# Optimization experiments

Hardware: AMD Instinct MI355X
Metric: run time of the kernel (lower is better)

The kernel has to match this reference:

```python
import jax, jax.numpy as jnp
import numpy as np

N_HARMONIC = 6
CONCAT = (3,)  # cfg.append_distance: concat embedding after this layer index
N_LAYERS = 8


def harmonic_embedding(x):
    # x: [N, 3] -> [N, 6*2*3 + 3] = [N, 39]
    freqs = 2.0 ** jnp.arange(N_HARMONIC, dtype=x.dtype)  # omega0 = 1.0, logspace
    embed = (x[..., None] * freqs).reshape(*x.shape[:-1], -1)  # [N, 18]
    return jnp.concatenate([jnp.sin(embed), jnp.cos(embed), x], axis=-1)


def setup_inputs() -> dict:
    key = jax.random.key(0)
    N, H, E = 262144, 256, 39
    ks = jax.random.split(key, 11)
    inp = {"points": jax.random.normal(ks[0], (N, 3), dtype=jnp.float32)}
    in_dims = [E, H, H, H, E + H, H, H, H]  # skip-concat before layer 4
    for i, d_in in enumerate(in_dims):
        scale = 1.0 / np.sqrt(d_in)
        inp[f"w{i}"] = jax.random.normal(ks[i + 1], (d_in, H), dtype=jnp.float32) * scale
        inp[f"b{i}"] = jnp.zeros((H,), dtype=jnp.float32)
    inp["wsdf"] = jax.random.normal(ks[9], (H, 1), dtype=jnp.float32) * (1.0 / np.sqrt(H))
    inp["bsdf"] = jnp.zeros((1,), dtype=jnp.float32)
    return inp


def reference(points, w0, b0, w1, b1, w2, b2, w3, b3, w4, b4, w5, b5, w6, b6, w7, b7, wsdf, bsdf):
    ws = [w0, w1, w2, w3, w4, w5, w6, w7]
    bs = [b0, b1, b2, b3, b4, b5, b6, b7]
    emb = harmonic_embedding(points.reshape(-1, 3))  # [N, 39]
    x = emb
    for i in range(N_LAYERS):
        x = jax.nn.relu(x @ ws[i] + bs[i])
        if i in CONCAT:
            x = jnp.concatenate([emb, x], axis=-1)  # torch.cat([add, xyz])
    return x @ wsdf + bsdf  # [N, 1] signed distance
```

## Files before the change

kernel.cpp:

```cpp
#include <hip/hip_runtime.h>
#include <hip/hip_fp16.h>

typedef _Float16 f16x8 __attribute__((ext_vector_type(8)));
typedef _Float16 f16x4 __attribute__((ext_vector_type(4)));
typedef _Float16 f16x2 __attribute__((ext_vector_type(2)));
typedef float    f32x16 __attribute__((ext_vector_type(16)));
typedef float    f32x4 __attribute__((ext_vector_type(4)));

#define SH 264
#define SE 56
#define PTS 64

struct LayerPtrs {
  const float* w[8];
  const float* b[8];
};

__global__ void prep_weights(LayerPtrs P, f16x8* __restrict__ wf) {
  int gid = blockIdx.x * 256 + threadIdx.x;
  if (gid >= 60416) return;
  const int OFF[9] = {0,1536,9728,17920,26112,35840,44032,52224,60416};
  int l = 0;
  while (gid >= OFF[l+1]) ++l;
  int f = gid - OFF[l];
  int lane = f & 63;
  int t = f >> 6;
  int mtile = t & 7;
  int kc = t >> 3;
  int col = mtile * 32 + (lane & 31);
  int kb  = (lane >> 5) * 8;
  const float* w = P.w[l];
  f16x8 v;
#pragma unroll
  for (int j = 0; j < 8; ++j) {
    float x = 0.f;
    if (l == 4) {
      if (kc < 3) {
        int k = kc * 16 + kb + j;
        if (k < 39) x = w[k * 256 + col];
      } else {
        int k = (kc - 3) * 16 + kb + j;
        x = w[(39 + k) * 256 + col];
      }
    } else if (l == 0) {
      int k = kc * 16 + kb + j;
      if (k < 39) x = w[k * 256 + col];
    } else {
      int k = kc * 16 + kb + j;
      x = w[k * 256 + col];
    }
    v[j] = (_Float16)x;
  }
  wf[gid] = v;
}

#define MFMA __builtin_amdgcn_mfma_f32_32x32x16_f16

__device__ __forceinline__ void aload2(f16x8& d0, f16x8& d1, const f16x8* p) {
  asm volatile("global_load_dwordx4 %0, %2, off\n\t"
               "global_load_dwordx4 %1, %2, off offset:1024"
               : "=&v"(d0), "=&v"(d1)
               : "v"(p));
}

__device__ __forceinline__ void mfma4(f16x8 a0, f16x8 a1, f16x8 v0, f16x8 v1,
                                      f32x16 acc[2][2]) {
  acc[0][0] = MFMA(a0, v0, acc[0][0], 0, 0, 0);
  acc[0][1] = MFMA(a0, v1, acc[0][1], 0, 0, 0);
  acc[1][0] = MFMA(a1, v0, acc[1][0], 0, 0, 0);
  acc[1][1] = MFMA(a1, v1, acc[1][1], 0, 0, 0);
}

__device__ __forceinline__ void mfma4_z(f16x8 a0, f16x8 a1, f16x8 v0, f16x8 v1,
                                        f32x16 acc[2][2]) {
  const f32x16 z = {};
  acc[0][0] = MFMA(a0, v0, z, 0, 0, 0);
  acc[0][1] = MFMA(a0, v1, z, 0, 0, 0);
  acc[1][0] = MFMA(a1, v0, z, 0, 0, 0);
  acc[1][1] = MFMA(a1, v1, z, 0, 0, 0);
}

template<int NKC, bool FIRST, int RSTRIDE>
__device__ __forceinline__ void mm(const f16x8* __restrict__ wb,
                                   const char* __restrict__ r0,
                                   f32x16 acc[2][2]) {
  f16x8 a00, a01, b00, b01, c00, c01;
  aload2(a00, a01, wb);
  if (NKC > 1) aload2(b00, b01, wb + 512);
  if (NKC > 2) aload2(c00, c01, wb + 1024);
  f16x8 v0 = *(const f16x8*)(r0);
  f16x8 v1 = *(const f16x8*)(r0 + RSTRIDE);
#pragma unroll
  for (int kc = 0; kc < NKC; ++kc) {
    f16x8 na0, na1, nv0, nv1;
    if (kc + 3 < NKC) aload2(na0, na1, wb + (kc + 3) * 512);
    if (kc + 1 < NKC) {
      const char* rp = r0 + 32 * (kc + 1);
      nv0 = *(const f16x8*)(rp);
      nv1 = *(const f16x8*)(rp + RSTRIDE);
    }
    if (kc + 3 < NKC)      asm volatile("s_waitcnt vmcnt(6)");
    else if (kc + 2 < NKC) asm volatile("s_waitcnt vmcnt(4)");
    else if (kc + 1 < NKC) asm volatile("s_waitcnt vmcnt(2)");
    else                   asm volatile("s_waitcnt vmcnt(0)");
    __builtin_amdgcn_sched_barrier(0);
    if (FIRST && kc == 0) mfma4_z(a00, a01, v0, v1, acc);
    else                  mfma4 (a00, a01, v0, v1, acc);
    if (kc + 1 < NKC) {
      a00 = b00; a01 = b01; b00 = c00; b01 = c01;
      v0 = nv0; v1 = nv1;
    }
    if (kc + 3 < NKC) { c00 = na0; c01 = na1; }
  }
}

__device__ __forceinline__ f16x4 relu_cvt4(float a0, float a1, float a2, float a3) {
  f16x2 lo = __builtin_bit_cast(f16x2, __builtin_amdgcn_cvt_pkrtz(a0, a1));
  f16x2 hi = __builtin_bit_cast(f16x2, __builtin_amdgcn_cvt_pkrtz(a2, a3));
  union { f16x4 v; f16x2 h[2]; } u;
  u.h[0] = lo; u.h[1] = hi;
  f16x4 z = {};
  return __builtin_elementwise_max(u.v, z);
}

__device__ __forceinline__ void store_epi(f32x16 acc[2][2],
                                          const float* __restrict__ bias,
                                          int wg, int p0, int h,
                                          _Float16* __restrict__ Hw) {
#pragma unroll
  for (int mt = 0; mt < 2; ++mt) {
    int hb = wg * 64 + mt * 32 + 4 * h;
#pragma unroll
    for (int g = 0; g < 4; ++g) {
      f32x4 q = *(const f32x4*)&bias[hb + 8 * g];
#pragma unroll
      for (int nt = 0; nt < 2; ++nt) {
        f16x4 o = relu_cvt4(acc[mt][nt][4 * g + 0] + q[0],
                            acc[mt][nt][4 * g + 1] + q[1],
                            acc[mt][nt][4 * g + 2] + q[2],
                            acc[mt][nt][4 * g + 3] + q[3]);
        *(f16x4*)&Hw[(nt * 32 + p0) * SH + hb + 8 * g] = o;
      }
    }
  }
}

__device__ __forceinline__ void emb_channel(_Float16* __restrict__ Erow,
                                            int c, float x) {
  _Float16 sv[6], cv[6];
  float fr = 1.f;
#pragma unroll
  for (int k = 0; k < 6; ++k) {
    float e = x * fr;
    sv[k] = (_Float16)__sinf(e);
    cv[k] = (_Float16)__cosf(e);
    fr *= 2.f;
  }
#pragma unroll
  for (int k = 0; k < 6; k += 2) {
    f16x2 s2 = {sv[k], sv[k + 1]};
    f16x2 c2 = {cv[k], cv[k + 1]};
    *(f16x2*)&Erow[6 * c + k]      = s2;
    *(f16x2*)&Erow[18 + 6 * c + k] = c2;
  }
  Erow[36 + c] = (_Float16)x;
}

__global__ __launch_bounds__(256, 2)
void mlp_fused(const float* __restrict__ points,
               LayerPtrs P,
               const f16x8* __restrict__ wf,
               const float* __restrict__ wsdf,
               const float* __restrict__ bsdf,
               float* __restrict__ out) {
  __shared__ __align__(16) _Float16 Hs0[PTS * SH];
  __shared__ __align__(16) _Float16 Hs1[PTS * SH];
  __shared__ __align__(16) _Float16 Es[PTS * SE];
  const int tid = threadIdx.x;
  const int blk = blockIdx.x;

  const int lane = tid & 63;
  const int wg   = tid >> 6;
  const int p0   = lane & 31;
  const int h    = lane >> 5;

  const f16x8* wb = wf + wg * 128 + lane;

  {
    int p = tid & 63, part = tid >> 6;
    _Float16* Erow = &Es[p * SE];
    if (part < 3) {
      emb_channel(Erow, part, points[(blk * PTS + p) * 3 + part]);
    } else {
      Erow[39] = (_Float16)0.f;
      f16x4 z4 = {};
      *(f16x4*)&Erow[40] = z4;
      *(f16x4*)&Erow[44] = z4;
      *(f16x4*)&Erow[48] = z4;
      *(f16x4*)&Erow[52] = z4;
    }
  }
  __syncthreads();

  const char* h0R = (const char*)Hs0 + (p0 * SH + 8 * h) * 2;
  const char* h1R = (const char*)Hs1 + (p0 * SH + 8 * h) * 2;
  const char* eR  = (const char*)Es  + (p0 * SE + 8 * h) * 2;

  f32x16 acc[2][2];
  const int WOFF[8] = {0, 1536, 9728, 17920, 26112, 35840, 44032, 52224};

  mm<3, true, 32 * SE * 2>(wb, eR, acc);
  store_epi(acc, P.b[0], wg, p0, h, Hs0);
  __syncthreads();
  mm<16, true, 32 * SH * 2>(wb + WOFF[1], h0R, acc);
  store_epi(acc, P.b[1], wg, p0, h, Hs1);
  __syncthreads();
  mm<16, true, 32 * SH * 2>(wb + WOFF[2], h1R, acc);
  store_epi(acc, P.b[2], wg, p0, h, Hs0);
  __syncthreads();
  mm<16, true, 32 * SH * 2>(wb + WOFF[3], h0R, acc);
  store_epi(acc, P.b[3], wg, p0, h, Hs1);
  __syncthreads();
  mm<3, true, 32 * SE * 2>(wb + 26112, eR, acc);
  mm<16, false, 32 * SH * 2>(wb + 27648, h1R, acc);
  store_epi(acc, P.b[4], wg, p0, h, Hs0);
  __syncthreads();
  mm<16, true, 32 * SH * 2>(wb + WOFF[5], h0R, acc);
  store_epi(acc, P.b[5], wg, p0, h, Hs1);
  __syncthreads();
  mm<16, true, 32 * SH * 2>(wb + WOFF[6], h1R, acc);
  store_epi(acc, P.b[6], wg, p0, h, Hs0);
  __syncthreads();
  mm<16, true, 32 * SH * 2>(wb + WOFF[7], h0R, acc);
  {
    float part0 = 0.f, part1 = 0.f;
    const float* b7 = P.b[7];
#pragma unroll
    for (int mt = 0; mt < 2; ++mt) {
#pragma unroll
      for (int g = 0; g < 4; ++g) {
        int idx = wg * 64 + mt * 32 + 8 * g + 4 * h;
        f32x4 qb = *(const f32x4*)&b7[idx];
        f32x4 qw = *(const f32x4*)&wsdf[idx];
#pragma unroll
        for (int r = 0; r < 4; ++r) {
          part0 += fmaxf(acc[mt][0][4 * g + r] + qb[r], 0.f) * qw[r];
          part1 += fmaxf(acc[mt][1][4 * g + r] + qb[r], 0.f) * qw[r];
        }
      }
    }
    float* PB = (float*)Es;
    PB[(wg * 2 + h) * 64 + p0]      = part0;
    PB[(wg * 2 + h) * 64 + 32 + p0] = part1;
    __syncthreads();
    if (tid < PTS) {
      float s = bsdf[0];
#pragma unroll
      for (int j = 0; j < 8; ++j) s += PB[j * 64 + tid];
      out[blk * PTS + tid] = s;
    }
  }
}

extern "C" void kernel_launch(void* const* d_in, const int* in_sizes, int n_in,
                              void* d_out, int out_size, void* d_ws, size_t ws_size,
                              hipStream_t stream) {
  const float* points = (const float*)d_in[0];
  LayerPtrs P;
  for (int i = 0; i < 8; ++i) {
    P.w[i] = (const float*)d_in[1 + 2 * i];
    P.b[i] = (const float*)d_in[2 + 2 * i];
  }
  const float* wsdf = (const float*)d_in[17];
  const float* bsdf = (const float*)d_in[18];
  f16x8* wf = (f16x8*)d_ws;

  int N = in_sizes[0] / 3;
  prep_weights<<<236, 256, 0, stream>>>(P, wf);
  mlp_fused<<<N / PTS, 256, 0, stream>>>(points, P, wf, wsdf, bsdf, (float*)d_out);
}
```

Measured before the change: 318.6 us.

## Single-buffer activation LDS and raise occupancy to three blocks per CU

Replaces the ping-pong pair of activation buffers with one shared buffer, adding an extra barrier between each layer's matmul reads and the epilogue writes. This cuts LDS per block roughly in half so launch bounds can request three blocks per SM/CU instead of two. The cost is one more __syncthreads per layer, which serialises compute and store within a block, and a tighter register budget that may cause spills.

```diff
diff --git a/kernel.cpp b/kernel.cpp
--- a/kernel.cpp
+++ b/kernel.cpp
@@ -126,7 +126,7 @@
 __device__ __forceinline__ void store_epi(f32x16 acc[2][2],
                                           const float* __restrict__ bias,
                                           int wg, int p0, int h,
-                                          _Float16* __restrict__ Hw) {
+                                          _Float16* __restrict__ Hs) {
 #pragma unroll
   for (int mt = 0; mt < 2; ++mt) {
     int hb = wg * 64 + mt * 32 + 4 * h;
@@ -139,7 +139,7 @@
                             acc[mt][nt][4 * g + 1] + q[1],
                             acc[mt][nt][4 * g + 2] + q[2],
                             acc[mt][nt][4 * g + 3] + q[3]);
-        *(f16x4*)&Hw[(nt * 32 + p0) * SH + hb + 8 * g] = o;
+        *(f16x4*)&Hs[(nt * 32 + p0) * SH + hb + 8 * g] = o;
       }
     }
   }
@@ -166,15 +166,14 @@
   Erow[36 + c] = (_Float16)x;
 }
 
-__global__ __launch_bounds__(256, 2)
+__global__ __launch_bounds__(256, 3)
 void mlp_fused(const float* __restrict__ points,
                LayerPtrs P,
                const f16x8* __restrict__ wf,
                const float* __restrict__ wsdf,
                const float* __restrict__ bsdf,
                float* __restrict__ out) {
-  __shared__ __align__(16) _Float16 Hs0[PTS * SH];
-  __shared__ __align__(16) _Float16 Hs1[PTS * SH];
+  __shared__ __align__(16) _Float16 Hs[PTS * SH];
   __shared__ __align__(16) _Float16 Es[PTS * SE];
   const int tid = threadIdx.x;
   const int blk = blockIdx.x;
@@ -202,36 +201,41 @@
   }
   __syncthreads();
 
-  const char* h0R = (const char*)Hs0 + (p0 * SH + 8 * h) * 2;
-  const char* h1R = (const char*)Hs1 + (p0 * SH + 8 * h) * 2;
-  const char* eR  = (const char*)Es  + (p0 * SE + 8 * h) * 2;
+  const char* hR = (const char*)Hs + (p0 * SH + 8 * h) * 2;
+  const char* eR = (const char*)Es + (p0 * SE + 8 * h) * 2;
 
   f32x16 acc[2][2];
   const int WOFF[8] = {0, 1536, 9728, 17920, 26112, 35840, 44032, 52224};
 
   mm<3, true, 32 * SE * 2>(wb, eR, acc);
-  store_epi(acc, P.b[0], wg, p0, h, Hs0);
+  store_epi(acc, P.b[0], wg, p0, h, Hs);
   __syncthreads();
-  mm<16, true, 32 * SH * 2>(wb + WOFF[1], h0R, acc);
-  store_epi(acc, P.b[1], wg, p0, h, Hs1);
-  __syncthreads();
-  mm<16, true, 32 * SH * 2>(wb + WOFF[2], h1R, acc);
-  store_epi(acc, P.b[2], wg, p0, h, Hs0);
-  __syncthreads();
-  mm<16, true, 32 * SH * 2>(wb + WOFF[3], h0R, acc);
-  store_epi(acc, P.b[3], wg, p0, h, Hs1);
-  __syncthreads();
-  mm<3, true, 32 * SE * 2>(wb + 26112, eR, acc);
-  mm<16, false, 32 * SH * 2>(wb + 27648, h1R, acc);
-  store_epi(acc, P.b[4], wg, p0, h, Hs0);
-  __syncthreads();
-  mm<16, true, 32 * SH * 2>(wb + WOFF[5], h0R, acc);
-  store_epi(acc, P.b[5], wg, p0, h, Hs1);
-  __syncthreads();
-  mm<16, true, 32 * SH * 2>(wb + WOFF[6], h1R, acc);
-  store_epi(acc, P.b[6], wg, p0, h, Hs0);
-  __syncthreads();
-  mm<16, true, 32 * SH * 2>(wb + WOFF[7], h0R, acc);
+
+#pragma unroll
+  for (int l = 1; l < 4; ++l) {
+    mm<16, true, 32 * SH * 2>(wb + WOFF[l], hR, acc);
+    __syncthreads();
+    store_epi(acc, P.b[l], wg, p0, h, Hs);
+    __syncthreads();
+  }
+
+  {
+    mm<3, true, 32 * SE * 2>(wb + 26112, eR, acc);
+    mm<16, false, 32 * SH * 2>(wb + 27648, hR, acc);
+    __syncthreads();
+    store_epi(acc, P.b[4], wg, p0, h, Hs);
+    __syncthreads();
+  }
+
+#pragma unroll
+  for (int l = 5; l < 7; ++l) {
+    mm<16, true, 32 * SH * 2>(wb + WOFF[l], hR, acc);
+    __syncthreads();
+    store_epi(acc, P.b[l], wg, p0, h, Hs);
+    __syncthreads();
+  }
+
+  mm<16, true, 32 * SH * 2>(wb + WOFF[7], hR, acc);
   {
     float part0 = 0.f, part1 = 0.f;
     const float* b7 = P.b[7];
```

Result: slower. 327.5 us (+2.8%).
